# Kernel optimization log

Measured on AMD Instinct MI355X. Metric: run time of the kernel, lower is better.

The kernel has to match this reference:

```python
import jax, jax.numpy as jnp
import numpy as np
from jax import lax

DN = ('NCHW', 'OIHW', 'NCHW')

def binarize(w):
    # torch: w.sign().add(0.5).sign() maps w<0 -> -1, w>=0 -> +1 (0 -> +1)
    return jnp.where(w < 0, -1.0, 1.0).astype(w.dtype)

def bconv(x, w, b, dil):
    wb = binarize(w)
    y = lax.conv_general_dilated(x, wb, window_strides=(1, 1), padding='SAME',
                                 rhs_dilation=dil, dimension_numbers=DN)
    return y + b[None, :, None, None]

def setup_inputs() -> dict:
    key = jax.random.key(0)
    ks = jax.random.split(key, 9)
    C = 256
    Co = C // 4
    x = jax.random.normal(ks[0], (16, C, 128, 128), dtype=jnp.float32)
    w1 = jax.random.normal(ks[1], (Co, C, 1, 5), dtype=jnp.float32) * 0.05
    w2 = jax.random.normal(ks[2], (Co, C, 1, 5), dtype=jnp.float32) * 0.05
    w3 = jax.random.normal(ks[3], (Co, C, 5, 1), dtype=jnp.float32) * 0.05
    w4 = jax.random.normal(ks[4], (Co, C, 5, 1), dtype=jnp.float32) * 0.05
    b1 = jax.random.normal(ks[5], (Co,), dtype=jnp.float32) * 0.01
    b2 = jax.random.normal(ks[6], (Co,), dtype=jnp.float32) * 0.01
    b3 = jax.random.normal(ks[7], (Co,), dtype=jnp.float32) * 0.01
    b4 = jax.random.normal(ks[8], (Co,), dtype=jnp.float32) * 0.01
    return {'x': x, 'w1': w1, 'b1': b1, 'w2': w2, 'b2': b2,
            'w3': w3, 'b3': b3, 'w4': w4, 'b4': b4}

def reference(x, w1, b1, w2, b2, w3, b3, w4, b4):
    out1 = bconv(x, w1, b1, (1, 1))  # (1,5) dil 1
    out2 = bconv(x, w2, b2, (2, 2))  # (1,5) dil 2 (only W dim matters, H kernel=1)
    out3 = bconv(x, w3, b3, (1, 1))  # (5,1) dil 1
    out4 = bconv(x, w4, b4, (2, 2))  # (5,1) dil 2
    return jnp.concatenate([out1, out2, out3, out4], axis=1)
```

## Files before the change

### kernel.cpp

```cpp
#include <hip/hip_runtime.h>

typedef _Float16 half8   __attribute__((ext_vector_type(8)));
typedef float    floatx4 __attribute__((ext_vector_type(4)));
typedef unsigned int uint4v __attribute__((ext_vector_type(4)));

#define HW      128
#define CIN     256
#define NCHUNK  8
#define HALO_W  24
#define HALO_H  16
#define NPIX    (HALO_W * HALO_H)
#define PITCH   20

__global__ void prep_weights(const float* __restrict__ w1,
                             const float* __restrict__ w2,
                             const float* __restrict__ w3,
                             const float* __restrict__ w4,
                             _Float16* __restrict__ wp)
{
    int idx  = blockIdx.x * 256 + threadIdx.x;
    int j    = idx & 7;
    int lane = (idx >> 3) & 63;
    int m    = (idx >> 9) & 3;
    int r3   = idx >> 11;
    int t    = r3 % 5;
    int r4   = r3 / 5;
    int chunk= r4 & 7;
    int b    = r4 >> 3;
    const float* w = (b == 0) ? w1 : (b == 1) ? w2 : (b == 2) ? w3 : w4;
    int co = m * 16 + (lane & 15);
    int ci = chunk * 32 + (lane >> 4) * 8 + j;
    float v = w[(co * 256 + ci) * 5 + t];
    wp[idx] = (v < 0.0f) ? (_Float16)(-1.0f) : (_Float16)(1.0f);
}

__global__ __launch_bounds__(512, 4)
void bconv_mfma(const float* __restrict__ x,
                const _Float16* __restrict__ wp,
                const float* __restrict__ bb1,
                const float* __restrict__ bb2,
                const float* __restrict__ bb3,
                const float* __restrict__ bb4,
                float* __restrict__ out)
{
    __shared__ __align__(16) unsigned int xs[2 * NPIX * PITCH];
    __shared__ float bias_s[256];

    const int tid = threadIdx.x;

    const int L  = blockIdx.x + 8 * (blockIdx.y + 16 * blockIdx.z);
    const int sw = (L & 7) * 256 + (L >> 3);
    const int w0t  = (sw & 7) * 16;
    const int h0t  = ((sw >> 3) & 15) * 8;
    const int nimg = sw >> 7;

    if (tid < 256) {
        int br = tid >> 6, i = tid & 63;
        const float* bp = (br == 0) ? bb1 : (br == 1) ? bb2 : (br == 2) ? bb3 : bb4;
        bias_s[tid] = bp[i];
    }

    const int lane   = tid & 63;
    const int wave   = tid >> 6;
    const int branch = wave >> 1;
    const int hhalf  = wave & 1;
    const int quad   = lane >> 4;
    const int wl     = lane & 15;
    const int dil    = (branch & 1) + 1;
    const bool horiz = (branch < 2);

    floatx4 acc[4][4];
    #pragma unroll
    for (int m = 0; m < 4; ++m)
        #pragma unroll
        for (int n = 0; n < 4; ++n)
            acc[m][n] = (floatx4){0.f, 0.f, 0.f, 0.f};

    auto stage = [&](int buf, int chunk) {
        unsigned int* xb = &xs[buf * (NPIX * PITCH)];
        #pragma unroll
        for (int s = 0; s < 3; ++s) {
            int idx = s * 512 + tid;
            int hh  = idx / 96;
            int rem = idx - hh * 96;
            int cb  = rem / 24;
            int ww  = rem - cb * 24;
            int hg  = h0t - 4 + hh;
            int wg  = w0t - 4 + ww;
            bool ok = (hg >= 0 && hg < HW && wg >= 0 && wg < HW);
            const float* p = x + (((nimg * CIN + chunk * 32 + cb * 8) * HW + hg) * HW + wg);
            float v[8];
            #pragma unroll
            for (int jj = 0; jj < 8; ++jj)
                v[jj] = ok ? p[jj * HW * HW] : 0.0f;
            uint4v u;
            #pragma unroll
            for (int jj = 0; jj < 4; ++jj)
                u[jj] = __builtin_bit_cast(unsigned int,
                            __builtin_amdgcn_cvt_pkrtz(v[2 * jj], v[2 * jj + 1]));
            *(uint4v*)&xb[(hh * HALO_W + ww) * PITCH + cb * 4] = u;
        }
    };

    stage(0, 0);

    for (int k = 0; k < NCHUNK; ++k) {
        __syncthreads();
        const unsigned int* xb  = &xs[(k & 1) * (NPIX * PITCH)];
        const _Float16*     wpc = wp + (branch * 8 + k) * (5 * 4 * 64 * 8);

        #pragma unroll
        for (int t = 0; t < 5; ++t) {
            half8 A[4];
            #pragma unroll
            for (int m = 0; m < 4; ++m)
                A[m] = *(const half8*)(wpc + ((t * 4 + m) * 64 + lane) * 8);
            #pragma unroll
            for (int n = 0; n < 4; ++n) {
                int hh, ww;
                if (horiz) { hh = hhalf * 4 + n + 4;                  ww = wl + 4 + (t - 2) * dil; }
                else       { hh = hhalf * 4 + n + 4 + (t - 2) * dil;  ww = wl + 4; }
                half8 B = *(const half8*)&xb[(hh * HALO_W + ww) * PITCH + quad * 4];
                #pragma unroll
                for (int m = 0; m < 4; ++m)
                    acc[m][n] = __builtin_amdgcn_mfma_f32_16x16x32_f16(A[m], B, acc[m][n], 0, 0, 0);
            }
        }

        if (k + 1 < NCHUNK) stage((k + 1) & 1, k + 1);
    }

    float bv[4][4];
    #pragma unroll
    for (int m = 0; m < 4; ++m)
        #pragma unroll
        for (int r = 0; r < 4; ++r)
            bv[m][r] = bias_s[branch * 64 + m * 16 + quad * 4 + r];

    #pragma unroll
    for (int m = 0; m < 4; ++m) {
        #pragma unroll
        for (int n = 0; n < 4; ++n) {
            int co   = branch * 64 + m * 16 + quad * 4;
            int h    = h0t + hhalf * 4 + n;
            int base = ((nimg * 256 + co) * HW + h) * HW + w0t + wl;
            #pragma unroll
            for (int r = 0; r < 4; ++r)
                out[base + r * HW * HW] = acc[m][n][r] + bv[m][r];
        }
    }
}

extern "C" void kernel_launch(void* const* d_in, const int* in_sizes, int n_in,
                              void* d_out, int out_size, void* d_ws, size_t ws_size,
                              hipStream_t stream)
{
    (void)in_sizes; (void)n_in; (void)out_size; (void)ws_size;
    const float* x  = (const float*)d_in[0];
    const float* w1 = (const float*)d_in[1];
    const float* b1 = (const float*)d_in[2];
    const float* w2 = (const float*)d_in[3];
    const float* b2 = (const float*)d_in[4];
    const float* w3 = (const float*)d_in[5];
    const float* b3 = (const float*)d_in[6];
    const float* w4 = (const float*)d_in[7];
    const float* b4 = (const float*)d_in[8];
    float*    out = (float*)d_out;
    _Float16* wp  = (_Float16*)d_ws;

    prep_weights<<<1280, 256, 0, stream>>>(w1, w2, w3, w4, wp);

    dim3 grid(128 / 16, 128 / 8, 16);
    bconv_mfma<<<grid, dim3(512), 0, stream>>>(x, wp, b1, b2, b3, b4, out);
}
```

Baseline: 731.3 us.

## Prefetch next input chunk into registers to overlap global loads with MFMA

Splits the input staging into a global-load phase into registers and an LDS-write phase. The load for chunk k+2 is issued before the compute of chunk k+1, so global memory latency can hide behind the MFMA work. The 24 extra live registers per thread are covered by relaxing the launch bounds from 4 to 2 blocks per SM, which lowers occupancy.

Measured after the change: 620.5 us. -15.2%, faster.

```diff
diff --git a/kernel.cpp b/kernel.cpp
--- a/kernel.cpp
+++ b/kernel.cpp
@@ -34,7 +34,7 @@
     wp[idx] = (v < 0.0f) ? (_Float16)(-1.0f) : (_Float16)(1.0f);
 }
 
-__global__ __launch_bounds__(512, 4)
+__global__ __launch_bounds__(512, 2)
 void bconv_mfma(const float* __restrict__ x,
                 const _Float16* __restrict__ wp,
                 const float* __restrict__ bb1,
@@ -76,8 +76,9 @@
         for (int n = 0; n < 4; ++n)
             acc[m][n] = (floatx4){0.f, 0.f, 0.f, 0.f};
 
-    auto stage = [&](int buf, int chunk) {
-        unsigned int* xb = &xs[buf * (NPIX * PITCH)];
+    float v[3][8];
+
+    auto stage_load = [&](int c) {
         #pragma unroll
         for (int s = 0; s < 3; ++s) {
             int idx = s * 512 + tid;
@@ -88,24 +89,37 @@
             int hg  = h0t - 4 + hh;
             int wg  = w0t - 4 + ww;
             bool ok = (hg >= 0 && hg < HW && wg >= 0 && wg < HW);
-            const float* p = x + (((nimg * CIN + chunk * 32 + cb * 8) * HW + hg) * HW + wg);
-            float v[8];
+            const float* p = x + (((nimg * CIN + c * 32 + cb * 8) * HW + hg) * HW + wg);
             #pragma unroll
             for (int jj = 0; jj < 8; ++jj)
-                v[jj] = ok ? p[jj * HW * HW] : 0.0f;
+                v[s][jj] = ok ? p[jj * HW * HW] : 0.0f;
+        }
+    };
+
+    auto stage_write = [&](int buf) {
+        unsigned int* xb = &xs[buf * (NPIX * PITCH)];
+        #pragma unroll
+        for (int s = 0; s < 3; ++s) {
+            int idx = s * 512 + tid;
+            int hh  = idx / 96;
+            int rem = idx - hh * 96;
+            int cb  = rem / 24;
+            int ww  = rem - cb * 24;
             uint4v u;
             #pragma unroll
             for (int jj = 0; jj < 4; ++jj)
                 u[jj] = __builtin_bit_cast(unsigned int,
-                            __builtin_amdgcn_cvt_pkrtz(v[2 * jj], v[2 * jj + 1]));
+                            __builtin_amdgcn_cvt_pkrtz(v[s][2 * jj], v[s][2 * jj + 1]));
             *(uint4v*)&xb[(hh * HALO_W + ww) * PITCH + cb * 4] = u;
         }
     };
 
-    stage(0, 0);
+    stage_load(0);
+    stage_write(0);
+    stage_load(1);
+    __syncthreads();
 
     for (int k = 0; k < NCHUNK; ++k) {
-        __syncthreads();
         const unsigned int* xb  = &xs[(k & 1) * (NPIX * PITCH)];
         const _Float16*     wpc = wp + (branch * 8 + k) * (5 * 4 * 64 * 8);
 
@@ -127,7 +141,11 @@
             }
         }
 
-        if (k + 1 < NCHUNK) stage((k + 1) & 1, k + 1);
+        if (k + 1 < NCHUNK) {
+            stage_write((k + 1) & 1);
+            if (k + 2 < NCHUNK) stage_load(k + 2);
+            __syncthreads();
+        }
     }
 
     float bv[4][4];
```
